# Kernel tuning notes

Measured on AMD Instinct MI355X. Metric: run time of the kernel, lower is better.

The kernel has to match this reference:

```python
import jax, jax.numpy as jnp
import numpy as np

B, C = 2048, 5000          # batchSize, classNum
LLR_REL = 0.9              # keep-rate; k = ceil(B*C*(1-llr_rel))
K = int(np.ceil(B * C * (1.0 - LLR_REL)))
MARGIN = 0.0


def _bce_with_logits(x, t):
    # elementwise BCEWithLogitsLoss (reduce=False): max(x,0) - x*t + log1p(exp(-|x|))
    return jnp.maximum(x, 0.0) - x * t + jnp.log1p(jnp.exp(-jnp.abs(x)))


def setup_inputs() -> dict:
    key = jax.random.key(0)
    k1, k2 = jax.random.split(key)
    inp = jax.random.normal(k1, (B, C), dtype=jnp.float32)
    # target in {-1, 0, +1}: -1 negative, 0 unobserved/ignored, +1 positive
    tgt = (jax.random.randint(k2, (B, C), 0, 3) - 1).astype(jnp.float32)
    return {"input": inp, "target": tgt, "k": K}


def reference(input, target, k):
    input = input.astype(jnp.float32)
    target = target.astype(jnp.float32)
    positive_mask = (target > MARGIN).astype(jnp.float32)
    negative_mask = (target < -MARGIN).astype(jnp.float32)
    positive_loss = _bce_with_logits(input, target)
    negative_loss = _bce_with_logits(-input, -target)
    unobserved_loss = negative_mask * negative_loss
    if k != 0:
        # k-th largest value of the flattened unobserved loss is the threshold
        topk_vals = jax.lax.top_k(unobserved_loss.reshape(-1), k)[0]
        topk_lossvalue = topk_vals[-1]
        loss_mask = (unobserved_loss < topk_lossvalue).astype(jnp.float32)
        negative_mask = negative_mask * loss_mask
    loss = positive_mask * positive_loss + negative_mask * negative_loss
    return loss
```

## Files before the change

### kernel.cpp

```cpp
#include <hip/hip_runtime.h>
#include <cstdint>


struct SelState {
    uint32_t prefix;
    uint32_t k_rem;
    uint32_t u_kth;
    float    thr_nl;
    uint32_t done;
};

#define GUARD 256u

__device__ __forceinline__ uint32_t xform(uint32_t b) {
    return ((int32_t)b < 0) ? ~b : (b | 0x80000000u);
}
__device__ __forceinline__ float unxform(uint32_t u) {
    uint32_t b = (u & 0x80000000u) ? (u ^ 0x80000000u) : ~u;
    return __uint_as_float(b);
}
__device__ __forceinline__ float neg_loss_precise(float x, float t) {
#pragma clang fp contract(off)
    return (fmaxf(-x, 0.0f) - x * t) + log1pf(expf(-fabsf(x)));
}

__device__ __forceinline__ void hist_quad(uint32_t* my, float4 xv, float4 tv) {
    uint32_t u0 = (tv.x < 0.0f) ? xform(__float_as_uint(xv.x)) : 0u;
    uint32_t u1 = (tv.y < 0.0f) ? xform(__float_as_uint(xv.y)) : 0u;
    uint32_t u2 = (tv.z < 0.0f) ? xform(__float_as_uint(xv.z)) : 0u;
    uint32_t u3 = (tv.w < 0.0f) ? xform(__float_as_uint(xv.w)) : 0u;
    if (u0) atomicAdd(&my[u0 >> 21], 1u);
    if (u1) atomicAdd(&my[u1 >> 21], 1u);
    if (u2) atomicAdd(&my[u2 >> 21], 1u);
    if (u3) atomicAdd(&my[u3 >> 21], 1u);
}

__global__ __launch_bounds__(256) void k1_hist(
        const float* __restrict__ x, const float* __restrict__ t,
        uint32_t* __restrict__ hist, int n) {
    __shared__ uint32_t lh[2 * 2049];
    for (int i = threadIdx.x; i < 2 * 2049; i += 256) lh[i] = 0;
    __syncthreads();
    uint32_t* my = &lh[(threadIdx.x & 1) * 2049];

    const float4* x4 = (const float4*)x;
    const float4* t4 = (const float4*)t;
    const int n4 = n >> 2;
    const int S = gridDim.x * 256;
    int i = blockIdx.x * 256 + threadIdx.x;
    for (; i + 3 * S < n4; i += 4 * S) {
        float4 xa = x4[i], xb = x4[i + S], xc = x4[i + 2 * S], xd = x4[i + 3 * S];
        float4 ta = t4[i], tb = t4[i + S], tc = t4[i + 2 * S], td = t4[i + 3 * S];
        hist_quad(my, xa, ta);
        hist_quad(my, xb, tb);
        hist_quad(my, xc, tc);
        hist_quad(my, xd, td);
    }
    for (; i < n4; i += S) {
        float4 xa = x4[i], ta = t4[i];
        hist_quad(my, xa, ta);
    }
    if (blockIdx.x == 0) {
        for (int j = (n4 << 2) + threadIdx.x; j < n; j += 256) {
            uint32_t u = (t[j] < 0.0f) ? xform(__float_as_uint(x[j])) : 0u;
            if (u) atomicAdd(&my[u >> 21], 1u);
        }
    }
    __syncthreads();
    for (int b = threadIdx.x; b < 2048; b += 256) {
        uint32_t c = lh[b] + lh[2049 + b];
        if (c) atomicAdd(&hist[b], c);
    }
}

__global__ __launch_bounds__(256) void scan1(
        const uint32_t* __restrict__ hist, SelState* __restrict__ st,
        const int* __restrict__ kptr) {
    __shared__ uint32_t part[256];
    const int tid = threadIdx.x;
    uint32_t cnt[8];
    uint32_t lsum = 0;
#pragma unroll
    for (int j = 0; j < 8; ++j) { cnt[j] = hist[tid * 8 + j]; lsum += cnt[j]; }
    part[tid] = lsum;
    __syncthreads();
    for (int off = 1; off < 256; off <<= 1) {
        uint32_t add = (tid + off < 256) ? part[tid + off] : 0u;
        __syncthreads();
        part[tid] += add;
        __syncthreads();
    }
    const uint32_t total = part[0];
    int kk = *kptr;
    uint32_t k = (kk > 0) ? (uint32_t)kk : 0u;
    if (k == 0u) {
        if (tid == 0) { st->u_kth = 0xFFFFFFFFu; st->thr_nl = __int_as_float(0x7F800000); st->done = 1u; }
        return;
    }
    if (k > total) {
        if (tid == 0) { st->u_kth = 0u; st->thr_nl = 0.0f; st->done = 1u; }
        return;
    }
    uint32_t A = (tid < 255) ? part[tid + 1] : 0u;
#pragma unroll
    for (int j = 7; j >= 0; --j) {
        uint32_t c = cnt[j];
        if (A < k && k <= A + c) {
            st->prefix = (uint32_t)(tid * 8 + j);
            st->k_rem = k - A;
        }
        A += c;
    }
}

__device__ __forceinline__ void cnt_quad(uint32_t* __restrict__ h21, uint32_t pref,
                                         float4 xv, float4 tv) {
    uint32_t u0 = (tv.x < 0.0f) ? xform(__float_as_uint(xv.x)) : 0u;
    uint32_t u1 = (tv.y < 0.0f) ? xform(__float_as_uint(xv.y)) : 0u;
    uint32_t u2 = (tv.z < 0.0f) ? xform(__float_as_uint(xv.z)) : 0u;
    uint32_t u3 = (tv.w < 0.0f) ? xform(__float_as_uint(xv.w)) : 0u;
    if (u0 && (u0 >> 21) == pref) atomicAdd(&h21[u0 & 0x1FFFFFu], 1u);
    if (u1 && (u1 >> 21) == pref) atomicAdd(&h21[u1 & 0x1FFFFFu], 1u);
    if (u2 && (u2 >> 21) == pref) atomicAdd(&h21[u2 & 0x1FFFFFu], 1u);
    if (u3 && (u3 >> 21) == pref) atomicAdd(&h21[u3 & 0x1FFFFFu], 1u);
}

__global__ __launch_bounds__(256) void k2_hist21(
        const float* __restrict__ x, const float* __restrict__ t,
        uint32_t* __restrict__ h21, const SelState* __restrict__ st, int n) {
    __shared__ uint32_t s_pref, s_done;
    if (threadIdx.x == 0) { s_pref = st->prefix; s_done = st->done; }
    __syncthreads();
    if (s_done) return;
    const uint32_t pref = s_pref;

    const float4* x4 = (const float4*)x;
    const float4* t4 = (const float4*)t;
    const int n4 = n >> 2;
    const int S = gridDim.x * 256;
    int i = blockIdx.x * 256 + threadIdx.x;
    for (; i + 3 * S < n4; i += 4 * S) {
        float4 xa = x4[i], xb = x4[i + S], xc = x4[i + 2 * S], xd = x4[i + 3 * S];
        float4 ta = t4[i], tb = t4[i + S], tc = t4[i + 2 * S], td = t4[i + 3 * S];
        cnt_quad(h21, pref, xa, ta);
        cnt_quad(h21, pref, xb, tb);
        cnt_quad(h21, pref, xc, tc);
        cnt_quad(h21, pref, xd, td);
    }
    for (; i < n4; i += S) {
        float4 xa = x4[i], ta = t4[i];
        cnt_quad(h21, pref, xa, ta);
    }
    if (blockIdx.x == 0) {
        for (int j = (n4 << 2) + threadIdx.x; j < n; j += 256) {
            uint32_t u = (t[j] < 0.0f) ? xform(__float_as_uint(x[j])) : 0u;
            if (u && (u >> 21) == pref) atomicAdd(&h21[u & 0x1FFFFFu], 1u);
        }
    }
}

__global__ __launch_bounds__(256) void scan2a(
        const uint32_t* __restrict__ h21, uint32_t* __restrict__ csums,
        const SelState* __restrict__ st) {
    __shared__ uint32_t red[256];
    __shared__ uint32_t s_done;
    if (threadIdx.x == 0) s_done = st->done;
    __syncthreads();
    if (s_done) return;
    const uint4* b4 = (const uint4*)(h21 + (size_t)blockIdx.x * 2048);
    uint32_t s = 0;
    for (int j = threadIdx.x; j < 512; j += 256) {
        uint4 v = b4[j];
        s += v.x + v.y + v.z + v.w;
    }
    red[threadIdx.x] = s;
    __syncthreads();
    for (int off = 128; off > 0; off >>= 1) {
        if (threadIdx.x < off) red[threadIdx.x] += red[threadIdx.x + off];
        __syncthreads();
    }
    if (threadIdx.x == 0) csums[blockIdx.x] = red[0];
}

__global__ __launch_bounds__(256) void scan2b(
        const uint32_t* __restrict__ h21, const uint32_t* __restrict__ csums,
        SelState* __restrict__ st) {
    __shared__ uint32_t part[256];
    __shared__ uint32_t sel[2];
    __shared__ SelState sst;
    const int tid = threadIdx.x;
    if (tid == 0) sst = *st;
    __syncthreads();
    if (sst.done) return;
    const uint32_t k = sst.k_rem;

    uint32_t c4[4];
    uint32_t lsum = 0;
#pragma unroll
    for (int j = 0; j < 4; ++j) { c4[j] = csums[tid * 4 + j]; lsum += c4[j]; }
    part[tid] = lsum;
    __syncthreads();
    for (int off = 1; off < 256; off <<= 1) {
        uint32_t add = (tid + off < 256) ? part[tid + off] : 0u;
        __syncthreads();
        part[tid] += add;
        __syncthreads();
    }
    uint32_t A = (tid < 255) ? part[tid + 1] : 0u;
#pragma unroll
    for (int j = 3; j >= 0; --j) {
        uint32_t c = c4[j];
        if (A < k && k <= A + c) { sel[0] = (uint32_t)(tid * 4 + j); sel[1] = k - A; }
        A += c;
    }
    __syncthreads();
    const uint32_t chunk = sel[0];
    const uint32_t k2 = sel[1];
    __syncthreads();

    const uint32_t* base = h21 + (size_t)chunk * 2048;
    uint32_t b8[8];
    lsum = 0;
#pragma unroll
    for (int j = 0; j < 8; ++j) { b8[j] = base[tid * 8 + j]; lsum += b8[j]; }
    part[tid] = lsum;
    __syncthreads();
    for (int off = 1; off < 256; off <<= 1) {
        uint32_t add = (tid + off < 256) ? part[tid + off] : 0u;
        __syncthreads();
        part[tid] += add;
        __syncthreads();
    }
    A = (tid < 255) ? part[tid + 1] : 0u;
#pragma unroll
    for (int j = 7; j >= 0; --j) {
        uint32_t c = b8[j];
        if (A < k2 && k2 <= A + c) {
            uint32_t u = (sst.prefix << 21) | (chunk * 2048u + (uint32_t)(tid * 8 + j));
            st->u_kth = u;
            st->thr_nl = neg_loss_precise(unxform(u), -1.0f);
            st->done = 1u;
        }
        A += c;
    }
}

__device__ __forceinline__ float fin1(float xx, float tt, uint32_t ukth, float thr) {
    float lp = __logf(1.0f + __expf(-fabsf(xx)));
    float v = 0.0f;
    if (tt > 0.0f) {
        v = fmaxf(xx, 0.0f) - xx * tt + lp;
    } else if (tt < 0.0f) {
        uint32_t u = xform(__float_as_uint(xx));
        bool keep = u < ukth;
        if (keep && (ukth - u) < GUARD)
            keep = neg_loss_precise(xx, tt) < thr;
        if (keep) v = fmaxf(-xx, 0.0f) - xx * tt + lp;
    }
    return v;
}

__device__ __forceinline__ float4 fin_quad(float4 xv, float4 tv, uint32_t ukth, float thr) {
    float4 r;
    r.x = fin1(xv.x, tv.x, ukth, thr);
    r.y = fin1(xv.y, tv.y, ukth, thr);
    r.z = fin1(xv.z, tv.z, ukth, thr);
    r.w = fin1(xv.w, tv.w, ukth, thr);
    return r;
}

__global__ __launch_bounds__(256) void k_final(
        const float* __restrict__ x, const float* __restrict__ t,
        const SelState* __restrict__ st, float* __restrict__ out, int n) {
    const uint32_t ukth = st->u_kth;
    const float thr = st->thr_nl;
    const float4* x4 = (const float4*)x;
    const float4* t4 = (const float4*)t;
    float4* o4 = (float4*)out;
    const int n4 = n >> 2;
    const int S = gridDim.x * 256;
    int i = blockIdx.x * 256 + threadIdx.x;
    for (; i + 3 * S < n4; i += 4 * S) {
        float4 xa = x4[i], xb = x4[i + S], xc = x4[i + 2 * S], xd = x4[i + 3 * S];
        float4 ta = t4[i], tb = t4[i + S], tc = t4[i + 2 * S], td = t4[i + 3 * S];
        o4[i]         = fin_quad(xa, ta, ukth, thr);
        o4[i + S]     = fin_quad(xb, tb, ukth, thr);
        o4[i + 2 * S] = fin_quad(xc, tc, ukth, thr);
        o4[i + 3 * S] = fin_quad(xd, td, ukth, thr);
    }
    for (; i < n4; i += S) {
        float4 xa = x4[i], ta = t4[i];
        o4[i] = fin_quad(xa, ta, ukth, thr);
    }
    if (blockIdx.x == 0) {
        for (int j = (n4 << 2) + threadIdx.x; j < n; j += 256) {
            out[j] = fin1(x[j], t[j], ukth, thr);
        }
    }
}

extern "C" void kernel_launch(void* const* d_in, const int* in_sizes, int n_in,
                              void* d_out, int out_size, void* d_ws, size_t ws_size,
                              hipStream_t stream) {
    const float* x = (const float*)d_in[0];
    const float* t = (const float*)d_in[1];
    const int* kptr = (const int*)d_in[2];
    float* out = (float*)d_out;
    const int n = in_sizes[0];
    if (n <= 0) return;

    char* ws = (char*)d_ws;
    uint32_t* hist1 = (uint32_t*)(ws + 0);
    uint32_t* csums = (uint32_t*)(ws + 8192);
    SelState* st    = (SelState*)(ws + 12288);
    uint32_t* h21   = (uint32_t*)(ws + 16384);

    hipMemsetAsync(d_ws, 0, 16384 + (size_t)(1u << 21) * 4u, stream);

    const int n4 = n >> 2;
    int work = (n4 + 255) / 256;
    if (work < 1) work = 1;
    int grid = work < 1024 ? work : 1024;

    k1_hist  <<<grid, 256, 0, stream>>>(x, t, hist1, n);
    scan1    <<<1, 256, 0, stream>>>(hist1, st, kptr);
    k2_hist21<<<grid, 256, 0, stream>>>(x, t, h21, st, n);
    scan2a   <<<1024, 256, 0, stream>>>(h21, csums, st);
    scan2b   <<<1, 256, 0, stream>>>(h21, csums, st);
    k_final  <<<grid, 256, 0, stream>>>(x, t, st, out, n);
}
```

Baseline: 177.3 us.

## Compact negative keys in first pass so second histogram pass reads only them

The first histogram kernel now also writes the transformed keys of negative-target elements into per-block segments in workspace, using wave-ballot compaction with one atomic per wave. The second histogram pass then reads only these compacted keys instead of rereading both full input arrays, which roughly cuts its reads to a third. In exchange the first pass does extra global writes and ballot work, and there is a fallback path when the workspace is too small. The final kernel grid is also raised to 2048 blocks.

Measured after the change: 203.1 us. +14.6%, slower.

```diff
diff --git a/kernel.cpp b/kernel.cpp
--- a/kernel.cpp
+++ b/kernel.cpp
@@ -24,7 +24,25 @@
     return (fmaxf(-x, 0.0f) - x * t) + log1pf(expf(-fabsf(x)));
 }
 
-__device__ __forceinline__ void hist_quad(uint32_t* my, float4 xv, float4 tv) {
+__device__ __forceinline__ void emit(uint32_t u, uint32_t* __restrict__ seg,
+                                     uint32_t* __restrict__ bcount) {
+    unsigned long long m = __ballot(u != 0u);
+    if (m) {
+        const int lane = threadIdx.x & 63;
+        const int leader = __ffsll((unsigned long long)m) - 1;
+        uint32_t base = 0;
+        if (lane == leader) base = atomicAdd(bcount, (uint32_t)__popcll(m));
+        base = __shfl(base, leader);
+        if (u) {
+            uint32_t off = (uint32_t)__popcll(m & ((1ULL << lane) - 1ULL));
+            seg[base + off] = u;
+        }
+    }
+}
+
+__device__ __forceinline__ void hist_quad(uint32_t* my, float4 xv, float4 tv,
+                                          uint32_t* __restrict__ seg,
+                                          uint32_t* __restrict__ bcount) {
     uint32_t u0 = (tv.x < 0.0f) ? xform(__float_as_uint(xv.x)) : 0u;
     uint32_t u1 = (tv.y < 0.0f) ? xform(__float_as_uint(xv.y)) : 0u;
     uint32_t u2 = (tv.z < 0.0f) ? xform(__float_as_uint(xv.z)) : 0u;
@@ -33,15 +51,24 @@
     if (u1) atomicAdd(&my[u1 >> 21], 1u);
     if (u2) atomicAdd(&my[u2 >> 21], 1u);
     if (u3) atomicAdd(&my[u3 >> 21], 1u);
+    if (seg) {
+        emit(u0, seg, bcount);
+        emit(u1, seg, bcount);
+        emit(u2, seg, bcount);
+        emit(u3, seg, bcount);
+    }
 }
 
 __global__ __launch_bounds__(256) void k1_hist(
         const float* __restrict__ x, const float* __restrict__ t,
-        uint32_t* __restrict__ hist, int n) {
+        uint32_t* __restrict__ hist, uint32_t* __restrict__ segs,
+        uint32_t* __restrict__ blockcount, uint32_t seg_cap, int n) {
     __shared__ uint32_t lh[2 * 2049];
     for (int i = threadIdx.x; i < 2 * 2049; i += 256) lh[i] = 0;
     __syncthreads();
     uint32_t* my = &lh[(threadIdx.x & 1) * 2049];
+    uint32_t* seg = segs ? segs + (size_t)blockIdx.x * seg_cap : nullptr;
+    uint32_t* bc = segs ? &blockcount[blockIdx.x] : nullptr;
 
     const float4* x4 = (const float4*)x;
     const float4* t4 = (const float4*)t;
@@ -51,19 +78,20 @@
     for (; i + 3 * S < n4; i += 4 * S) {
         float4 xa = x4[i], xb = x4[i + S], xc = x4[i + 2 * S], xd = x4[i + 3 * S];
         float4 ta = t4[i], tb = t4[i + S], tc = t4[i + 2 * S], td = t4[i + 3 * S];
-        hist_quad(my, xa, ta);
-        hist_quad(my, xb, tb);
-        hist_quad(my, xc, tc);
-        hist_quad(my, xd, td);
+        hist_quad(my, xa, ta, seg, bc);
+        hist_quad(my, xb, tb, seg, bc);
+        hist_quad(my, xc, tc, seg, bc);
+        hist_quad(my, xd, td, seg, bc);
     }
     for (; i < n4; i += S) {
         float4 xa = x4[i], ta = t4[i];
-        hist_quad(my, xa, ta);
+        hist_quad(my, xa, ta, seg, bc);
     }
     if (blockIdx.x == 0) {
         for (int j = (n4 << 2) + threadIdx.x; j < n; j += 256) {
             uint32_t u = (t[j] < 0.0f) ? xform(__float_as_uint(x[j])) : 0u;
             if (u) atomicAdd(&my[u >> 21], 1u);
+            if (seg) emit(u, seg, bc);
         }
     }
     __syncthreads();
@@ -113,48 +141,53 @@
     }
 }
 
-__device__ __forceinline__ void cnt_quad(uint32_t* __restrict__ h21, uint32_t pref,
-                                         float4 xv, float4 tv) {
-    uint32_t u0 = (tv.x < 0.0f) ? xform(__float_as_uint(xv.x)) : 0u;
-    uint32_t u1 = (tv.y < 0.0f) ? xform(__float_as_uint(xv.y)) : 0u;
-    uint32_t u2 = (tv.z < 0.0f) ? xform(__float_as_uint(xv.z)) : 0u;
-    uint32_t u3 = (tv.w < 0.0f) ? xform(__float_as_uint(xv.w)) : 0u;
-    if (u0 && (u0 >> 21) == pref) atomicAdd(&h21[u0 & 0x1FFFFFu], 1u);
-    if (u1 && (u1 >> 21) == pref) atomicAdd(&h21[u1 & 0x1FFFFFu], 1u);
-    if (u2 && (u2 >> 21) == pref) atomicAdd(&h21[u2 & 0x1FFFFFu], 1u);
-    if (u3 && (u3 >> 21) == pref) atomicAdd(&h21[u3 & 0x1FFFFFu], 1u);
-}
-
 __global__ __launch_bounds__(256) void k2_hist21(
         const float* __restrict__ x, const float* __restrict__ t,
-        uint32_t* __restrict__ h21, const SelState* __restrict__ st, int n) {
+        const uint32_t* __restrict__ segs, const uint32_t* __restrict__ blockcount,
+        uint32_t seg_cap, uint32_t* __restrict__ h21,
+        const SelState* __restrict__ st, int n) {
     __shared__ uint32_t s_pref, s_done;
     if (threadIdx.x == 0) { s_pref = st->prefix; s_done = st->done; }
     __syncthreads();
     if (s_done) return;
     const uint32_t pref = s_pref;
 
-    const float4* x4 = (const float4*)x;
-    const float4* t4 = (const float4*)t;
-    const int n4 = n >> 2;
-    const int S = gridDim.x * 256;
-    int i = blockIdx.x * 256 + threadIdx.x;
-    for (; i + 3 * S < n4; i += 4 * S) {
-        float4 xa = x4[i], xb = x4[i + S], xc = x4[i + 2 * S], xd = x4[i + 3 * S];
-        float4 ta = t4[i], tb = t4[i + S], tc = t4[i + 2 * S], td = t4[i + 3 * S];
-        cnt_quad(h21, pref, xa, ta);
-        cnt_quad(h21, pref, xb, tb);
-        cnt_quad(h21, pref, xc, tc);
-        cnt_quad(h21, pref, xd, td);
-    }
-    for (; i < n4; i += S) {
-        float4 xa = x4[i], ta = t4[i];
-        cnt_quad(h21, pref, xa, ta);
-    }
-    if (blockIdx.x == 0) {
-        for (int j = (n4 << 2) + threadIdx.x; j < n; j += 256) {
-            uint32_t u = (t[j] < 0.0f) ? xform(__float_as_uint(x[j])) : 0u;
-            if (u && (u >> 21) == pref) atomicAdd(&h21[u & 0x1FFFFFu], 1u);
+    if (segs) {
+        const uint32_t cnt = blockcount[blockIdx.x];
+        const uint32_t* seg = segs + (size_t)blockIdx.x * seg_cap;
+        uint32_t j = threadIdx.x;
+        for (; j + 768u < cnt; j += 1024u) {
+            uint32_t a = seg[j], b = seg[j + 256], c = seg[j + 512], d = seg[j + 768];
+            if ((a >> 21) == pref) atomicAdd(&h21[a & 0x1FFFFFu], 1u);
+            if ((b >> 21) == pref) atomicAdd(&h21[b & 0x1FFFFFu], 1u);
+            if ((c >> 21) == pref) atomicAdd(&h21[c & 0x1FFFFFu], 1u);
+            if ((d >> 21) == pref) atomicAdd(&h21[d & 0x1FFFFFu], 1u);
+        }
+        for (; j < cnt; j += 256u) {
+            uint32_t a = seg[j];
+            if ((a >> 21) == pref) atomicAdd(&h21[a & 0x1FFFFFu], 1u);
+        }
+    } else {
+        const float4* x4 = (const float4*)x;
+        const float4* t4 = (const float4*)t;
+        const int n4 = n >> 2;
+        const int S = gridDim.x * 256;
+        for (int i = blockIdx.x * 256 + threadIdx.x; i < n4; i += S) {
+            float4 xv = x4[i], tv = t4[i];
+            uint32_t u0 = (tv.x < 0.0f) ? xform(__float_as_uint(xv.x)) : 0u;
+            uint32_t u1 = (tv.y < 0.0f) ? xform(__float_as_uint(xv.y)) : 0u;
+            uint32_t u2 = (tv.z < 0.0f) ? xform(__float_as_uint(xv.z)) : 0u;
+            uint32_t u3 = (tv.w < 0.0f) ? xform(__float_as_uint(xv.w)) : 0u;
+            if (u0 && (u0 >> 21) == pref) atomicAdd(&h21[u0 & 0x1FFFFFu], 1u);
+            if (u1 && (u1 >> 21) == pref) atomicAdd(&h21[u1 & 0x1FFFFFu], 1u);
+            if (u2 && (u2 >> 21) == pref) atomicAdd(&h21[u2 & 0x1FFFFFu], 1u);
+            if (u3 && (u3 >> 21) == pref) atomicAdd(&h21[u3 & 0x1FFFFFu], 1u);
+        }
+        if (blockIdx.x == 0) {
+            for (int j = (n4 << 2) + threadIdx.x; j < n; j += 256) {
+                uint32_t u = (t[j] < 0.0f) ? xform(__float_as_uint(x[j])) : 0u;
+                if (u && (u >> 21) == pref) atomicAdd(&h21[u & 0x1FFFFFu], 1u);
+            }
         }
     }
 }
@@ -313,19 +346,28 @@
     uint32_t* hist1 = (uint32_t*)(ws + 0);
     uint32_t* csums = (uint32_t*)(ws + 8192);
     SelState* st    = (SelState*)(ws + 12288);
-    uint32_t* h21   = (uint32_t*)(ws + 16384);
-
-    hipMemsetAsync(d_ws, 0, 16384 + (size_t)(1u << 21) * 4u, stream);
+    uint32_t* bcnt  = (uint32_t*)(ws + 16384);
+    uint32_t* h21   = (uint32_t*)(ws + 32768);
+    const size_t h21_end = 32768 + (size_t)(1u << 21) * 4u;
 
     const int n4 = n >> 2;
     int work = (n4 + 255) / 256;
     if (work < 1) work = 1;
-    int grid = work < 1024 ? work : 1024;
-
-    k1_hist  <<<grid, 256, 0, stream>>>(x, t, hist1, n);
+    int grid1 = work < 1024 ? work : 1024;
+    int gridF = work < 2048 ? work : 2048;
+
+    const int S1 = grid1 * 256;
+    const uint32_t iters = (uint32_t)((n4 + S1 - 1) / S1);
+    const uint32_t seg_cap = iters * 4u * 256u + 4u;
+    const size_t need = h21_end + (size_t)seg_cap * 4u * (size_t)grid1;
+    uint32_t* segs = (ws_size >= need) ? (uint32_t*)(ws + h21_end) : nullptr;
+
+    hipMemsetAsync(d_ws, 0, h21_end, stream);
+
+    k1_hist  <<<grid1, 256, 0, stream>>>(x, t, hist1, segs, bcnt, seg_cap, n);
     scan1    <<<1, 256, 0, stream>>>(hist1, st, kptr);
-    k2_hist21<<<grid, 256, 0, stream>>>(x, t, h21, st, n);
+    k2_hist21<<<grid1, 256, 0, stream>>>(x, t, segs, bcnt, seg_cap, h21, st, n);
     scan2a   <<<1024, 256, 0, stream>>>(h21, csums, st);
     scan2b   <<<1, 256, 0, stream>>>(h21, csums, st);
-    k_final  <<<grid, 256, 0, stream>>>(x, t, st, out, n);
-}
+    k_final  <<<gridF, 256, 0, stream>>>(x, t, st, out, n);
+}
```
